# Performance work log

Measured on AMD Instinct MI355X. Metric: run time of the kernel, lower is better.

Reference implementation:

```python
import jax, jax.numpy as jnp
import numpy as np

D = 1024
H = 16
HD = D // H
EPS = 1e-5

def _layernorm(x, g, b):
    xf = x.astype(jnp.float32)
    mu = jnp.mean(xf, axis=-1, keepdims=True)
    var = jnp.mean(jnp.square(xf - mu), axis=-1, keepdims=True)
    return ((xf - mu) * jax.lax.rsqrt(var + EPS) * g + b).astype(x.dtype)

def setup_inputs() -> dict:
    key = jax.random.key(0)
    ks = jax.random.split(key, 12)
    B, S = 4, 1024
    s_in = 1.0 / np.sqrt(D)
    inp = {
        "x": jax.random.normal(ks[0], (B, S, D), dtype=jnp.float32),
        "in_proj_w": jax.random.normal(ks[1], (3 * D, D), dtype=jnp.float32) * s_in,
        "in_proj_b": jnp.zeros((3 * D,), dtype=jnp.float32),
        "out_w": jax.random.normal(ks[2], (D, D), dtype=jnp.float32) * s_in,
        "out_b": jnp.zeros((D,), dtype=jnp.float32),
        "ln1_g": jnp.ones((D,), dtype=jnp.float32),
        "ln1_b": jnp.zeros((D,), dtype=jnp.float32),
        "fc_w": jax.random.normal(ks[3], (4 * D, D), dtype=jnp.float32) * s_in,
        "fc_b": jnp.zeros((4 * D,), dtype=jnp.float32),
        "proj_w": jax.random.normal(ks[4], (D, 4 * D), dtype=jnp.float32) * (1.0 / np.sqrt(4 * D)),
        "proj_b": jnp.zeros((D,), dtype=jnp.float32),
        "ln2_g": jnp.ones((D,), dtype=jnp.float32),
        "ln2_b": jnp.zeros((D,), dtype=jnp.float32),
    }
    return inp

def reference(x, in_proj_w, in_proj_b, out_w, out_b, ln1_g, ln1_b,
              fc_w, fc_b, proj_w, proj_b, ln2_g, ln2_b):
    B, S, _ = x.shape
    scaling = float(HD) ** -0.5
    # --- attention sublayer ---
    h = _layernorm(x, ln1_g, ln1_b)
    qkv = h @ in_proj_w.T + in_proj_b              # [B,S,3D]
    q, k, v = jnp.split(qkv, 3, axis=-1)
    q = (q * scaling).reshape(B, S, H, HD).transpose(0, 2, 1, 3)  # [B,H,S,hd]
    k = k.reshape(B, S, H, HD).transpose(0, 2, 1, 3)
    v = v.reshape(B, S, H, HD).transpose(0, 2, 1, 3)
    attn = jax.nn.softmax(jnp.einsum('bhqd,bhkd->bhqk', q, k), axis=-1)
    o = jnp.einsum('bhqk,bhkd->bhqd', attn, v).transpose(0, 2, 1, 3).reshape(B, S, D)
    x = x + o @ out_w.T + out_b
    # --- MLP sublayer (QuickGELU) ---
    h = _layernorm(x, ln2_g, ln2_b)
    u = h @ fc_w.T + fc_b                          # [B,S,4D]
    u = u * jax.nn.sigmoid(1.702 * u)
    x = x + u @ proj_w.T + proj_b
    return x
```

## Files before the change

kernel.cpp:

```cpp
#include <hip/hip_runtime.h>
#include <math.h>

#define D_MODEL 1024
#define SEQ     1024
#define BATCH   4
#define NTOK    (BATCH * SEQ)

typedef __bf16 bf16;
using bfrag = __attribute__((ext_vector_type(8))) __bf16;
using ffrag = __attribute__((ext_vector_type(4))) float;

__device__ __forceinline__ ffrag mfma16(bfrag a, bfrag b, ffrag c) {
  return __builtin_amdgcn_mfma_f32_16x16x32_bf16(a, b, c, 0, 0, 0);
}

__device__ __forceinline__ void gload_lds16(const void* g, void* l) {
  __builtin_amdgcn_global_load_lds(
      (const __attribute__((address_space(1))) void*)g,
      (__attribute__((address_space(3))) void*)l, 16, 0, 0);
}

__global__ void convert_all(const float* __restrict__ s0, bf16* __restrict__ d0, int n0,
                            const float* __restrict__ s1, bf16* __restrict__ d1, int n1,
                            const float* __restrict__ s2, bf16* __restrict__ d2, int n2,
                            const float* __restrict__ s3, bf16* __restrict__ d3, int n3,
                            float scale, int limit0) {
  const float* src; bf16* dst; int n; int limit = 0;
  switch (blockIdx.y) {
    case 0: src = s0; dst = d0; n = n0; limit = limit0; break;
    case 1: src = s1; dst = d1; n = n1; break;
    case 2: src = s2; dst = d2; n = n2; break;
    default: src = s3; dst = d3; n = n3; break;
  }
  int i = blockIdx.x * blockDim.x + threadIdx.x;
  const int stride = gridDim.x * blockDim.x;
  for (; i < n; i += stride) {
    float4 v = ((const float4*)src)[i];
    float sc = (i < limit) ? scale : 1.0f;
    bf16* d = dst + (size_t)i * 4;
    d[0] = (bf16)(v.x * sc); d[1] = (bf16)(v.y * sc);
    d[2] = (bf16)(v.z * sc); d[3] = (bf16)(v.w * sc);
  }
}

__global__ void scale_bias(const float* __restrict__ src, float* __restrict__ dst,
                           int n, int limit, float scale) {
  int i = blockIdx.x * blockDim.x + threadIdx.x;
  if (i < n) dst[i] = src[i] * (i < limit ? scale : 1.0f);
}

__global__ __launch_bounds__(256) void ln_row(const float* __restrict__ x,
                                              const float* __restrict__ gamma,
                                              const float* __restrict__ beta,
                                              bf16* __restrict__ out) {
  const int row = blockIdx.x, tid = threadIdx.x;
  const float4 v = ((const float4*)(x + (size_t)row * D_MODEL))[tid];
  float s  = v.x + v.y + v.z + v.w;
  float ss = v.x * v.x + v.y * v.y + v.z * v.z + v.w * v.w;
#pragma unroll
  for (int off = 32; off >= 1; off >>= 1) {
    s  += __shfl_xor(s, off);
    ss += __shfl_xor(ss, off);
  }
  __shared__ float rs[4], rss[4];
  const int w = tid >> 6;
  if ((tid & 63) == 0) { rs[w] = s; rss[w] = ss; }
  __syncthreads();
  s  = rs[0] + rs[1] + rs[2] + rs[3];
  ss = rss[0] + rss[1] + rss[2] + rss[3];
  const float mu   = s * (1.0f / D_MODEL);
  const float var  = ss * (1.0f / D_MODEL) - mu * mu;
  const float rstd = rsqrtf(var + 1e-5f);
  const float4 gv = ((const float4*)gamma)[tid];
  const float4 bv = ((const float4*)beta)[tid];
  bf16* o = out + (size_t)row * D_MODEL + tid * 4;
  o[0] = (bf16)((v.x - mu) * rstd * gv.x + bv.x);
  o[1] = (bf16)((v.y - mu) * rstd * gv.y + bv.y);
  o[2] = (bf16)((v.z - mu) * rstd * gv.z + bv.z);
  o[3] = (bf16)((v.w - mu) * rstd * gv.w + bv.w);
}

template <int EPI>
__global__ __launch_bounds__(256, 2) void gemm_bt(
    const bf16* __restrict__ A, const bf16* __restrict__ B,
    const float* __restrict__ bias, const float* __restrict__ resid,
    float* __restrict__ outF, bf16* __restrict__ outB,
    int M, int N, int K) {
  __shared__ bf16 As[2][128 * 32];
  __shared__ bf16 Bs[2][128 * 32];
  const int tid = threadIdx.x;
  const int lane = tid & 63, w = tid >> 6;
  const int wm = w >> 1, wn = w & 1;
  const int ql = lane & 15, lg = lane >> 4;
  const int m0 = blockIdx.x * 128, n0 = blockIdx.y * 128;

  ffrag acc[4][4];
#pragma unroll
  for (int i = 0; i < 4; i++)
#pragma unroll
    for (int j = 0; j < 4; j++) acc[i][j] = ffrag{0.f, 0.f, 0.f, 0.f};

  const int r0 = tid >> 2;
  const int jsw = (tid & 3) ^ (r0 & 3);
  const bf16* a0 = A + (size_t)(m0 + r0) * K + jsw * 8;
  const bf16* a1 = A + (size_t)(m0 + 64 + r0) * K + jsw * 8;
  const bf16* b0 = B + (size_t)(n0 + r0) * K + jsw * 8;
  const bf16* b1 = B + (size_t)(n0 + 64 + r0) * K + jsw * 8;
  const int lo = w * 512;

  auto STAGE = [&](int bs, int kk) {
    gload_lds16(a0 + kk, &As[bs][lo]);
    gload_lds16(a1 + kk, &As[bs][2048 + lo]);
    gload_lds16(b0 + kk, &Bs[bs][lo]);
    gload_lds16(b1 + kk, &Bs[bs][2048 + lo]);
  };

  STAGE(0, 0);
  __syncthreads();

  int cur = 0;
  for (int k0 = 0; k0 < K; k0 += 32) {
    if (k0 + 32 < K) STAGE(cur ^ 1, k0 + 32);
    bfrag af[4], bfr[4];
#pragma unroll
    for (int i = 0; i < 4; i++) {
      const int row = wm * 64 + i * 16 + ql;
      af[i] = *(const bfrag*)&As[cur][row * 32 + ((lg ^ (row & 3)) * 8)];
    }
#pragma unroll
    for (int j = 0; j < 4; j++) {
      const int row = wn * 64 + j * 16 + ql;
      bfr[j] = *(const bfrag*)&Bs[cur][row * 32 + ((lg ^ (row & 3)) * 8)];
    }
#pragma unroll
    for (int i = 0; i < 4; i++)
#pragma unroll
      for (int j = 0; j < 4; j++)
        acc[i][j] = mfma16(af[i], bfr[j], acc[i][j]);
    __syncthreads();
    cur ^= 1;
  }

#pragma unroll
  for (int i = 0; i < 4; i++) {
    const int row = m0 + wm * 64 + i * 16 + lg * 4;
#pragma unroll
    for (int j = 0; j < 4; j++) {
      const int col = n0 + wn * 64 + j * 16 + ql;
      const float bv = bias[col];
#pragma unroll
      for (int r = 0; r < 4; r++) {
        float v = acc[i][j][r] + bv;
        const size_t idx = (size_t)(row + r) * N + col;
        if (EPI == 0) {
          outB[idx] = (bf16)v;
        } else if (EPI == 1) {
          outF[idx] = v + resid[idx];
        } else {
          outB[idx] = (bf16)(v / (1.0f + __expf(-1.702f * v)));
        }
      }
    }
  }
}

template <int EPI>
__global__ __launch_bounds__(256, 4) void gemm_bt64(
    const bf16* __restrict__ A, const bf16* __restrict__ B,
    const float* __restrict__ bias, const float* __restrict__ resid,
    float* __restrict__ outF, bf16* __restrict__ outB,
    int M, int N, int K) {
  __shared__ bf16 As[2][64 * 64];
  __shared__ bf16 Bs[2][64 * 64];
  const int tid = threadIdx.x;
  const int lane = tid & 63, w = tid >> 6;
  const int wm = w >> 1, wn = w & 1;
  const int ql = lane & 15, lg = lane >> 4;
  const int m0 = blockIdx.x * 64, n0 = blockIdx.y * 64;

  ffrag acc[2][2];
#pragma unroll
  for (int i = 0; i < 2; i++)
#pragma unroll
    for (int j = 0; j < 2; j++) acc[i][j] = ffrag{0.f, 0.f, 0.f, 0.f};

  const int r0 = tid >> 3;
  const int jsw = ((tid & 7) ^ (r0 & 7)) * 8;
  const bf16* a0 = A + (size_t)(m0 + r0) * K + jsw;
  const bf16* a1 = A + (size_t)(m0 + 32 + r0) * K + jsw;
  const bf16* b0 = B + (size_t)(n0 + r0) * K + jsw;
  const bf16* b1 = B + (size_t)(n0 + 32 + r0) * K + jsw;
  const int lo = tid * 8;

  auto STAGE = [&](int bs, int kk) {
    gload_lds16(a0 + kk, &As[bs][lo]);
    gload_lds16(a1 + kk, &As[bs][2048 + lo]);
    gload_lds16(b0 + kk, &Bs[bs][lo]);
    gload_lds16(b1 + kk, &Bs[bs][2048 + lo]);
  };

  STAGE(0, 0);
  __syncthreads();

  int cur = 0;
  for (int k0 = 0; k0 < K; k0 += 64) {
    if (k0 + 64 < K) STAGE(cur ^ 1, k0 + 64);
    bfrag af[2][2], bfr[2][2];
#pragma unroll
    for (int i = 0; i < 2; i++) {
      const int row = wm * 32 + i * 16 + ql;
      const int r7 = row & 7;
#pragma unroll
      for (int kc = 0; kc < 2; kc++)
        af[i][kc] = *(const bfrag*)&As[cur][row * 64 + (((lg + 4 * kc) ^ r7) * 8)];
    }
#pragma unroll
    for (int j = 0; j < 2; j++) {
      const int row = wn * 32 + j * 16 + ql;
      const int r7 = row & 7;
#pragma unroll
      for (int kc = 0; kc < 2; kc++)
        bfr[j][kc] = *(const bfrag*)&Bs[cur][row * 64 + (((lg + 4 * kc) ^ r7) * 8)];
    }
#pragma unroll
    for (int kc = 0; kc < 2; kc++)
#pragma unroll
      for (int i = 0; i < 2; i++)
#pragma unroll
        for (int j = 0; j < 2; j++)
          acc[i][j] = mfma16(af[i][kc], bfr[j][kc], acc[i][j]);
    __syncthreads();
    cur ^= 1;
  }

#pragma unroll
  for (int i = 0; i < 2; i++) {
    const int row = m0 + wm * 32 + i * 16 + lg * 4;
#pragma unroll
    for (int j = 0; j < 2; j++) {
      const int col = n0 + wn * 32 + j * 16 + ql;
      const float bv = bias[col];
#pragma unroll
      for (int r = 0; r < 4; r++) {
        float v = acc[i][j][r] + bv;
        const size_t idx = (size_t)(row + r) * N + col;
        if (EPI == 0) {
          outB[idx] = (bf16)v;
        } else if (EPI == 1) {
          outF[idx] = v + resid[idx];
        } else {
          outB[idx] = (bf16)(v / (1.0f + __expf(-1.702f * v)));
        }
      }
    }
  }
}

__global__ __launch_bounds__(256) void transpose_v(const bf16* __restrict__ qkv,
                                                   bf16* __restrict__ vt) {
  __shared__ bf16 T[64 * 66];
  const int tid = threadIdx.x;
  const int bh = blockIdx.y, b = bh >> 4, h = bh & 15;
  const int s0 = blockIdx.x * 64;
  const bf16* src = qkv + (size_t)b * SEQ * 3072 + 2048 + h * 64;

  const int sl = tid >> 3, c = tid & 7;
#pragma unroll
  for (int p = 0; p < 2; p++) {
    const int s = sl + p * 32;
    const bfrag v = *(const bfrag*)(src + (size_t)(s0 + s) * 3072 + c * 8);
#pragma unroll
    for (int e = 0; e < 8; e++) T[s * 66 + c * 8 + e] = v[e];
  }
  __syncthreads();
  bf16* dst = vt + (size_t)bh * 64 * 1024;
#pragma unroll
  for (int p = 0; p < 2; p++) {
    const int d = sl + p * 32;
    bfrag o;
#pragma unroll
    for (int e = 0; e < 8; e++) o[e] = T[(c * 8 + e) * 66 + d];
    *(bfrag*)(dst + (size_t)d * 1024 + s0 + c * 8) = o;
  }
}

__global__ __launch_bounds__(256, 2) void flash_attn(const bf16* __restrict__ qkv,
                                                     const bf16* __restrict__ vt,
                                                     bf16* __restrict__ o) {
  __shared__ bf16 Kl[64 * 64];
  __shared__ bf16 Vl[64 * 64];
  __shared__ bf16 Pl[4 * 16 * 72];
  const int tid = threadIdx.x, lane = tid & 63, wid = tid >> 6;
  const int ql = lane & 15, lg = lane >> 4;
  const int bh = blockIdx.y, b = bh >> 4, h = bh & 15;
  const int qrow0 = blockIdx.x * 64 + wid * 16;
  const size_t headq = (size_t)b * SEQ * 3072 + (size_t)h * 64;

  const bf16* qp = qkv + headq + (size_t)(qrow0 + ql) * 3072 + lg * 8;
  const bfrag q0 = *(const bfrag*)qp;
  const bfrag q1 = *(const bfrag*)(qp + 32);

  float mrun[4], lrun[4];
  ffrag oacc[4];
#pragma unroll
  for (int r = 0; r < 4; r++) { mrun[r] = -3e38f; lrun[r] = 0.0f; }
#pragma unroll
  for (int f = 0; f < 4; f++) oacc[f] = ffrag{0.f, 0.f, 0.f, 0.f};

  const int sr = tid >> 3, sc = tid & 7;
  const int gsw = (sc ^ (sr & 7)) * 8;
  const bf16* kp0 = qkv + headq + 1024 + (size_t)sr * 3072 + gsw;
  const bf16* kp1 = kp0 + (size_t)32 * 3072;
  const bf16* vp0 = vt + (size_t)bh * 64 * 1024 + (size_t)sr * 1024 + gsw;
  const bf16* vp1 = vp0 + (size_t)32 * 1024;
  bf16* kl0 = Kl + tid * 8;
  bf16* kl1 = Kl + 2048 + tid * 8;
  bf16* vl0 = Vl + tid * 8;
  bf16* vl1 = Vl + 2048 + tid * 8;
  bf16* Pw = Pl + wid * 1152;

  for (int kt = 0; kt < SEQ; kt += 64) {
    gload_lds16(kp0, kl0); gload_lds16(kp1, kl1);
    gload_lds16(vp0, vl0); gload_lds16(vp1, vl1);
    kp0 += (size_t)64 * 3072; kp1 += (size_t)64 * 3072;
    vp0 += 64; vp1 += 64;
    __syncthreads();

    ffrag sa[4];
    __builtin_amdgcn_s_setprio(1);
#pragma unroll
    for (int sub = 0; sub < 4; sub++) {
      const int krow = sub * 16 + ql;
      const int r7 = krow & 7;
      const bfrag kf0 = *(const bfrag*)&Kl[krow * 64 + ((lg ^ r7) * 8)];
      const bfrag kf1 = *(const bfrag*)&Kl[krow * 64 + (((lg + 4) ^ r7) * 8)];
      ffrag s4 = ffrag{0.f, 0.f, 0.f, 0.f};
      s4 = mfma16(q0, kf0, s4);
      s4 = mfma16(q1, kf1, s4);
      sa[sub] = s4;
    }
    __builtin_amdgcn_s_setprio(0);

#pragma unroll
    for (int r = 0; r < 4; r++) {
      float mx = fmaxf(fmaxf(sa[0][r], sa[1][r]), fmaxf(sa[2][r], sa[3][r]));
      mx = fmaxf(mx, __shfl_xor(mx, 1));
      mx = fmaxf(mx, __shfl_xor(mx, 2));
      mx = fmaxf(mx, __shfl_xor(mx, 4));
      mx = fmaxf(mx, __shfl_xor(mx, 8));
      const float mnew = fmaxf(mrun[r], mx);
      const float corr = __expf(mrun[r] - mnew);
      float p[4], srow = 0.f;
#pragma unroll
      for (int sub = 0; sub < 4; sub++) {
        p[sub] = __expf(sa[sub][r] - mnew);
        srow += p[sub];
      }
      srow += __shfl_xor(srow, 1);
      srow += __shfl_xor(srow, 2);
      srow += __shfl_xor(srow, 4);
      srow += __shfl_xor(srow, 8);
      lrun[r] = lrun[r] * corr + srow;
      mrun[r] = mnew;
#pragma unroll
      for (int f = 0; f < 4; f++) oacc[f][r] *= corr;
      bf16* prow = Pw + (lg * 4 + r) * 72;
#pragma unroll
      for (int sub = 0; sub < 4; sub++) prow[sub * 16 + ql] = (bf16)p[sub];
    }

    const bfrag pa0 = *(const bfrag*)&Pw[ql * 72 + lg * 8];
    const bfrag pa1 = *(const bfrag*)&Pw[ql * 72 + 32 + lg * 8];
    __builtin_amdgcn_s_setprio(1);
#pragma unroll
    for (int f = 0; f < 4; f++) {
      const int vrow = f * 16 + ql;
      const int r7 = vrow & 7;
      const bfrag vf0 = *(const bfrag*)&Vl[vrow * 64 + ((lg ^ r7) * 8)];
      const bfrag vf1 = *(const bfrag*)&Vl[vrow * 64 + (((lg + 4) ^ r7) * 8)];
      oacc[f] = mfma16(pa0, vf0, oacc[f]);
      oacc[f] = mfma16(pa1, vf1, oacc[f]);
    }
    __builtin_amdgcn_s_setprio(0);
    __syncthreads();
  }

#pragma unroll
  for (int f = 0; f < 4; f++) {
#pragma unroll
    for (int r = 0; r < 4; r++) {
      const size_t orow = (size_t)b * SEQ + qrow0 + lg * 4 + r;
      o[orow * 1024 + h * 64 + f * 16 + ql] = (bf16)(oacc[f][r] / lrun[r]);
    }
  }
}

extern "C" void kernel_launch(void* const* d_in, const int* in_sizes, int n_in,
                              void* d_out, int out_size, void* d_ws, size_t ws_size,
                              hipStream_t stream) {
  (void)in_sizes; (void)n_in; (void)out_size; (void)ws_size;
  const float* x      = (const float*)d_in[0];
  const float* in_w   = (const float*)d_in[1];
  const float* in_b   = (const float*)d_in[2];
  const float* out_w  = (const float*)d_in[3];
  const float* out_b  = (const float*)d_in[4];
  const float* ln1_g  = (const float*)d_in[5];
  const float* ln1_b  = (const float*)d_in[6];
  const float* fc_w   = (const float*)d_in[7];
  const float* fc_b   = (const float*)d_in[8];
  const float* proj_w = (const float*)d_in[9];
  const float* proj_b = (const float*)d_in[10];
  const float* ln2_g  = (const float*)d_in[11];
  const float* ln2_b  = (const float*)d_in[12];
  float* out = (float*)d_out;

  char* p = (char*)d_ws;
  auto alloc = [&](size_t bytes) { char* r = p; p += (bytes + 255) & ~255ull; return r; };
  bf16* w_qkv  = (bf16*)alloc((size_t)3072 * 1024 * 2);
  bf16* w_out  = (bf16*)alloc((size_t)1024 * 1024 * 2);
  bf16* w_fc   = (bf16*)alloc((size_t)4096 * 1024 * 2);
  bf16* w_proj = (bf16*)alloc((size_t)1024 * 4096 * 2);
  float* b_qkv = (float*)alloc((size_t)3072 * 4);
  bf16* hbuf   = (bf16*)alloc((size_t)NTOK * 1024 * 2);
  float* x2    = (float*)alloc((size_t)NTOK * 1024 * 4);
  bf16* qkv    = (bf16*)alloc((size_t)NTOK * 3072 * 2);
  bf16* aout   = (bf16*)alloc((size_t)NTOK * 1024 * 2);
  bf16* ubuf   = qkv;
  bf16* vtb    = (bf16*)x2;

  const float scaling = 0.125f;
  convert_all<<<dim3(1024, 4), 256, 0, stream>>>(
      in_w, w_qkv, 3072 * 1024 / 4,
      out_w, w_out, 1024 * 1024 / 4,
      fc_w, w_fc, 4096 * 1024 / 4,
      proj_w, w_proj, 4096 * 1024 / 4,
      scaling, 1024 * 1024 / 4);
  scale_bias<<<12, 256, 0, stream>>>(in_b, b_qkv, 3072, 1024, scaling);

  ln_row<<<NTOK, 256, 0, stream>>>(x, ln1_g, ln1_b, hbuf);
  gemm_bt<0><<<dim3(32, 24), 256, 0, stream>>>(hbuf, w_qkv, b_qkv, nullptr,
                                               nullptr, qkv, NTOK, 3072, 1024);
  transpose_v<<<dim3(16, 64), 256, 0, stream>>>(qkv, vtb);
  flash_attn<<<dim3(16, 64), 256, 0, stream>>>(qkv, vtb, aout);
  gemm_bt64<1><<<dim3(64, 16), 256, 0, stream>>>(aout, w_out, out_b, x,
                                                 x2, nullptr, NTOK, 1024, 1024);
  ln_row<<<NTOK, 256, 0, stream>>>(x2, ln2_g, ln2_b, hbuf);
  gemm_bt<2><<<dim3(32, 32), 256, 0, stream>>>(hbuf, w_fc, fc_b, nullptr,
                                               nullptr, ubuf, NTOK, 4096, 1024);
  gemm_bt64<1><<<dim3(64, 16), 256, 0, stream>>>(ubuf, w_proj, proj_b, x2,
                                                 out, nullptr, NTOK, 1024, 4096);
}
```

Before: 239.9 us.

## Widen flash-attention key tiles, read V from global, use lazy exp2 rescaling

The flash-attention kernel now processes 128 keys per iteration and stages only K in LDS. V fragments are loaded straight from the pre-transposed global buffer, which frees shared memory so launch bounds can target four blocks per CU. The softmax now works in base 2, with log2(e) folded into the query scaling, and skips the running-max rescale unless some row's max grows by more than 8. This trades fewer barriers and rescale passes for uncached global V loads and larger per-thread register use.

```diff
diff --git a/kernel.cpp b/kernel.cpp
--- a/kernel.cpp
+++ b/kernel.cpp
@@ -284,12 +284,11 @@
   }
 }
 
-__global__ __launch_bounds__(256, 2) void flash_attn(const bf16* __restrict__ qkv,
+__global__ __launch_bounds__(256, 4) void flash_attn(const bf16* __restrict__ qkv,
                                                      const bf16* __restrict__ vt,
                                                      bf16* __restrict__ o) {
-  __shared__ bf16 Kl[64 * 64];
-  __shared__ bf16 Vl[64 * 64];
-  __shared__ bf16 Pl[4 * 16 * 72];
+  __shared__ bf16 Kl[128 * 64];
+  __shared__ bf16 Pl[4 * 16 * 136];
   const int tid = threadIdx.x, lane = tid & 63, wid = tid >> 6;
   const int ql = lane & 15, lg = lane >> 4;
   const int bh = blockIdx.y, b = bh >> 4, h = bh & 15;
@@ -303,33 +302,26 @@
   float mrun[4], lrun[4];
   ffrag oacc[4];
 #pragma unroll
-  for (int r = 0; r < 4; r++) { mrun[r] = -3e38f; lrun[r] = 0.0f; }
+  for (int r = 0; r < 4; r++) { mrun[r] = -1e30f; lrun[r] = 0.0f; }
 #pragma unroll
   for (int f = 0; f < 4; f++) oacc[f] = ffrag{0.f, 0.f, 0.f, 0.f};
 
-  const int sr = tid >> 3, sc = tid & 7;
-  const int gsw = (sc ^ (sr & 7)) * 8;
-  const bf16* kp0 = qkv + headq + 1024 + (size_t)sr * 3072 + gsw;
-  const bf16* kp1 = kp0 + (size_t)32 * 3072;
-  const bf16* vp0 = vt + (size_t)bh * 64 * 1024 + (size_t)sr * 1024 + gsw;
-  const bf16* vp1 = vp0 + (size_t)32 * 1024;
-  bf16* kl0 = Kl + tid * 8;
-  bf16* kl1 = Kl + 2048 + tid * 8;
-  bf16* vl0 = Vl + tid * 8;
-  bf16* vl1 = Vl + 2048 + tid * 8;
-  bf16* Pw = Pl + wid * 1152;
-
-  for (int kt = 0; kt < SEQ; kt += 64) {
-    gload_lds16(kp0, kl0); gload_lds16(kp1, kl1);
-    gload_lds16(vp0, vl0); gload_lds16(vp1, vl1);
-    kp0 += (size_t)64 * 3072; kp1 += (size_t)64 * 3072;
-    vp0 += 64; vp1 += 64;
+  const int r0 = tid >> 3;
+  const int jsw = ((tid & 7) ^ (r0 & 7)) * 8;
+  const bf16* kp = qkv + headq + 1024 + (size_t)r0 * 3072 + jsw;
+  bf16* Pw = Pl + wid * 2176;
+  const bf16* vhead = vt + (size_t)bh * 64 * 1024;
+
+  for (int kt = 0; kt < SEQ; kt += 128) {
+#pragma unroll
+    for (int pp = 0; pp < 4; pp++)
+      gload_lds16(kp + (size_t)(kt + pp * 32) * 3072, &Kl[pp * 2048 + tid * 8]);
     __syncthreads();
 
-    ffrag sa[4];
+    ffrag sa[8];
     __builtin_amdgcn_s_setprio(1);
 #pragma unroll
-    for (int sub = 0; sub < 4; sub++) {
+    for (int sub = 0; sub < 8; sub++) {
       const int krow = sub * 16 + ql;
       const int r7 = krow & 7;
       const bfrag kf0 = *(const bfrag*)&Kl[krow * 64 + ((lg ^ r7) * 8)];
@@ -341,45 +333,63 @@
     }
     __builtin_amdgcn_s_setprio(0);
 
+    float lmax[4];
 #pragma unroll
     for (int r = 0; r < 4; r++) {
-      float mx = fmaxf(fmaxf(sa[0][r], sa[1][r]), fmaxf(sa[2][r], sa[3][r]));
-      mx = fmaxf(mx, __shfl_xor(mx, 1));
-      mx = fmaxf(mx, __shfl_xor(mx, 2));
-      mx = fmaxf(mx, __shfl_xor(mx, 4));
-      mx = fmaxf(mx, __shfl_xor(mx, 8));
-      const float mnew = fmaxf(mrun[r], mx);
-      const float corr = __expf(mrun[r] - mnew);
-      float p[4], srow = 0.f;
-#pragma unroll
-      for (int sub = 0; sub < 4; sub++) {
-        p[sub] = __expf(sa[sub][r] - mnew);
-        srow += p[sub];
+      float m = sa[0][r];
+#pragma unroll
+      for (int sub = 1; sub < 8; sub++) m = fmaxf(m, sa[sub][r]);
+      lmax[r] = m;
+    }
+    bool ok = (lmax[0] - mrun[0] <= 8.0f) && (lmax[1] - mrun[1] <= 8.0f) &&
+              (lmax[2] - mrun[2] <= 8.0f) && (lmax[3] - mrun[3] <= 8.0f);
+    if (!__all(ok)) {
+#pragma unroll
+      for (int r = 0; r < 4; r++) {
+        float mx = lmax[r];
+        mx = fmaxf(mx, __shfl_xor(mx, 1));
+        mx = fmaxf(mx, __shfl_xor(mx, 2));
+        mx = fmaxf(mx, __shfl_xor(mx, 4));
+        mx = fmaxf(mx, __shfl_xor(mx, 8));
+        const float mnew = fmaxf(mrun[r], mx);
+        const float corr = exp2f(mrun[r] - mnew);
+        lrun[r] *= corr;
+#pragma unroll
+        for (int f = 0; f < 4; f++) oacc[f][r] *= corr;
+        mrun[r] = mnew;
+      }
+    }
+#pragma unroll
+    for (int r = 0; r < 4; r++) {
+      float pv[8], srow = 0.f;
+#pragma unroll
+      for (int sub = 0; sub < 8; sub++) {
+        pv[sub] = exp2f(sa[sub][r] - mrun[r]);
+        srow += pv[sub];
       }
       srow += __shfl_xor(srow, 1);
       srow += __shfl_xor(srow, 2);
       srow += __shfl_xor(srow, 4);
       srow += __shfl_xor(srow, 8);
-      lrun[r] = lrun[r] * corr + srow;
-      mrun[r] = mnew;
-#pragma unroll
-      for (int f = 0; f < 4; f++) oacc[f][r] *= corr;
-      bf16* prow = Pw + (lg * 4 + r) * 72;
-#pragma unroll
-      for (int sub = 0; sub < 4; sub++) prow[sub * 16 + ql] = (bf16)p[sub];
-    }
-
-    const bfrag pa0 = *(const bfrag*)&Pw[ql * 72 + lg * 8];
-    const bfrag pa1 = *(const bfrag*)&Pw[ql * 72 + 32 + lg * 8];
+      lrun[r] += srow;
+      bf16* prow = Pw + (lg * 4 + r) * 136;
+#pragma unroll
+      for (int sub = 0; sub < 8; sub++) prow[sub * 16 + ql] = (bf16)pv[sub];
+    }
+
+    bfrag pa[4];
+#pragma unroll
+    for (int kc = 0; kc < 4; kc++)
+      pa[kc] = *(const bfrag*)&Pw[ql * 136 + kc * 32 + lg * 8];
     __builtin_amdgcn_s_setprio(1);
 #pragma unroll
     for (int f = 0; f < 4; f++) {
-      const int vrow = f * 16 + ql;
-      const int r7 = vrow & 7;
-      const bfrag vf0 = *(const bfrag*)&Vl[vrow * 64 + ((lg ^ r7) * 8)];
-      const bfrag vf1 = *(const bfrag*)&Vl[vrow * 64 + (((lg + 4) ^ r7) * 8)];
-      oacc[f] = mfma16(pa0, vf0, oacc[f]);
-      oacc[f] = mfma16(pa1, vf1, oacc[f]);
+      const bf16* vbase = vhead + (size_t)(f * 16 + ql) * 1024 + kt + lg * 8;
+#pragma unroll
+      for (int kc = 0; kc < 4; kc++) {
+        const bfrag vf = *(const bfrag*)(vbase + kc * 32);
+        oacc[f] = mfma16(pa[kc], vf, oacc[f]);
+      }
     }
     __builtin_amdgcn_s_setprio(0);
     __syncthreads();
@@ -428,7 +438,7 @@
   bf16* ubuf   = qkv;
   bf16* vtb    = (bf16*)x2;
 
-  const float scaling = 0.125f;
+  const float scaling = 0.125f * 1.44269504089f;
   convert_all<<<dim3(1024, 4), 256, 0, stream>>>(
       in_w, w_qkv, 3072 * 1024 / 4,
       out_w, w_out, 1024 * 1024 / 4,
```

New measurement: 256.8 us. 1.07x slower.
